# Optimization experiments

Hardware: AMD Instinct MI355X
Metric: run time of the kernel (lower is better)

The kernel has to match this reference:

```python
import jax, jax.numpy as jnp
import numpy as np

EPS_BN = 1e-5
EPS_SIM = 1e-8
PAD = 1
NUM_ITERS = 3


def capsule_conv2d(x, w):
    # x: [B, C, H, W]; w: [out_caps, in_caps, kh, kw, in_len, out_len]
    B, C, H, W = x.shape
    oc, ic, kh, kw, il, ol = w.shape
    # im2col patches, feature dim ordered (c, kh, kw) -> matches torch.unfold
    patches = jax.lax.conv_general_dilated_patches(
        x, (kh, kw), (1, 1), [(PAD, PAD), (PAD, PAD)])  # [B, C*kh*kw, H, W]
    N = H * W
    p = patches.reshape(B, ic, il, kh * kw, N)
    p = jnp.transpose(p, (0, 4, 1, 3, 2))  # [B, N, ic, kk, il]
    wf = w.reshape(oc, ic, kh * kw, il, ol)
    # per-patch capsule transform -> priors [B, N, oc, ic*kk, ol]
    priors = jnp.einsum('bnikl,oiklm->bnoikm', p, wf)
    priors = priors.reshape(B, N, oc, ic * kh * kw, ol)
    # k-means routing with Tonimoto similarity, 3 iterations, no squash
    out = priors.mean(axis=-2, keepdims=True)  # [B, N, oc, 1, ol]
    for _ in range(NUM_ITERS):
        dot = jnp.sum(priors * out, axis=-1, keepdims=True)
        n1 = jnp.sum(priors * priors, axis=-1, keepdims=True)
        n2 = jnp.sum(out * out, axis=-1, keepdims=True)
        logits = dot / jnp.maximum(n1 + n2 - dot, EPS_SIM)
        probs = jax.nn.softmax(logits, axis=-2)
        out = jnp.sum(probs * priors, axis=-2, keepdims=True)
    out = out[..., 0, :]                      # [B, N, oc, ol]
    out = out.reshape(B, H, W, oc * ol)       # channels = oc*ol
    return jnp.transpose(out, (0, 3, 1, 2))   # [B, C, H, W]


def batchnorm2d(x, gamma, beta):
    mean = x.mean(axis=(0, 2, 3), keepdims=True)
    var = x.var(axis=(0, 2, 3), keepdims=True)  # biased, as torch BN training fwd
    inv = jax.lax.rsqrt(var + EPS_BN)
    return gamma[None, :, None, None] * (x - mean) * inv + beta[None, :, None, None]


def setup_inputs() -> dict:
    key = jax.random.key(0)
    k0, k1, k2 = jax.random.split(key, 3)
    B, C, H, W = 2, 64, 96, 96
    IL = OL = 8
    x = jax.random.normal(k0, (B, C, H, W), jnp.float32)
    w1 = jax.random.normal(k1, (C // OL, C // IL, 3, 3, IL, OL), jnp.float32) * 0.1
    w2 = jax.random.normal(k2, (C // OL, C // OL, 3, 3, OL, OL), jnp.float32) * 0.1
    g1 = jnp.ones((C,), jnp.float32)
    b1 = jnp.zeros((C,), jnp.float32)
    g2 = jnp.ones((C,), jnp.float32)
    b2 = jnp.zeros((C,), jnp.float32)
    return {"x": x, "w1": w1, "g1": g1, "b1": b1, "w2": w2, "g2": g2, "b2": b2}


def reference(x, w1, g1, b1, w2, g2, b2):
    r = batchnorm2d(capsule_conv2d(x, w1), g1, b1)
    r = batchnorm2d(capsule_conv2d(r, w2), g2, b2)
    return x + r
```

## Files before the change

### kernel.cpp

```cpp
#include <hip/hip_runtime.h>
#include <hip/hip_bf16.h>

#define HW 9216
#define NPC 18432
#define NELEM 1179648
#define XSTR 72
#define PATCH_B 7776
#define XREC 12
#define XBUF_B (4*2*16*2*XREC*4)

typedef __attribute__((ext_vector_type(2))) float f32x2;
typedef __attribute__((ext_vector_type(4))) float f32x4v;
typedef __attribute__((ext_vector_type(8))) short short8v;

__device__ __forceinline__ int detect_is32(const unsigned short* __restrict__ w1u) {
    int lane = threadIdx.x & 63;
    int bad = 0;
    #pragma unroll
    for (int i = 0; i < 16; ++i) {
        unsigned short u = (unsigned short)(w1u[lane + i * 64] & 0x7FFF);
        bad |= (u >= 0x42C8);
    }
    return (__ballot(bad) != 0ULL) ? 1 : 0;
}

__device__ __forceinline__ float load_in(const void* p, int idx, int is32) {
    return is32 ? ((const float*)p)[idx]
                : __bfloat162float(((const __hip_bfloat16*)p)[idx]);
}

__device__ __forceinline__ float lo16(unsigned v) { return __int_as_float((int)(v << 16)); }
__device__ __forceinline__ float hi16(unsigned v) { return __int_as_float((int)(v & 0xFFFF0000u)); }
__device__ __forceinline__ unsigned pk2bf(float a, float b) {
    __hip_bfloat162 h = __float22bfloat162_rn(float2{a, b});
    return *(unsigned*)&h;
}

__device__ __forceinline__ float dotsq4(const f32x4v a) {
    float t = a[0] * a[0];
    t = fmaf(a[1], a[1], t);
    t = fmaf(a[2], a[2], t);
    t = fmaf(a[3], a[3], t);
    return t;
}
__device__ __forceinline__ float dot4(const f32x4v a, const float om[4]) {
    float t = a[0] * om[0];
    t = fmaf(a[1], om[1], t);
    t = fmaf(a[2], om[2], t);
    t = fmaf(a[3], om[3], t);
    return t;
}

__launch_bounds__(256)
__global__ void prep_kernel(const void* __restrict__ x,
                            const void* __restrict__ w1, const void* __restrict__ w2,
                            __hip_bfloat16* __restrict__ xt,
                            __hip_bfloat16* __restrict__ Bfr1,
                            __hip_bfloat16* __restrict__ Bfr2,
                            float* __restrict__ statz) {
    __shared__ float tile[64 * 33];
    const int bid = blockIdx.x;
    if (bid < 576) {
        const int is32 = detect_is32((const unsigned short*)w1);
        int xb = bid % 3, y = (bid / 3) % 96, b = bid / 288;
        int x0 = xb * 32;
        for (int e = threadIdx.x; e < 2048; e += 256) {
            int xl = e & 31, c = e >> 5;
            tile[c * 33 + xl] = load_in(x, ((b * 64 + c) * 96 + y) * 96 + x0 + xl, is32);
        }
        __syncthreads();
        for (int f = threadIdx.x; f < 1024; f += 256) {
            int c2 = f & 31, xl = f >> 5;
            float a = tile[(2 * c2) * 33 + xl];
            float c = tile[(2 * c2 + 1) * 33 + xl];
            *(unsigned*)&xt[((b * 96 + y) * 96 + x0 + xl) * 64 + 2 * c2] = pk2bf(a, c);
        }
    } else if (bid < 720) {
        const int is32 = detect_is32((const unsigned short*)w1);
        int t = (bid - 576) * 256 + threadIdx.x;
        int layer = t / 18432;
        int r = t - layer * 18432;
        int lane = r & 63;
        int fi = r >> 6;
        int h = fi & 1, g = (fi >> 1) & 1;
        int kq = fi >> 2;
        int k = kq % 9, o = kq / 9;
        int dy = k / 3, dx = k % 3;
        int quad = lane >> 4, colhi = (lane >> 3) & 1, m = lane & 7;
        int heff = h ^ (m >> 2);
        int act = (quad == 2 * heff + colhi);
        int i = g * 4 + 2 * heff + colhi;
        const void* w = layer ? w2 : w1;
        __hip_bfloat16* dst = layer ? Bfr2 : Bfr1;
        #pragma unroll
        for (int j = 0; j < 8; ++j) {
            float v = act ? load_in(w, ((((o * 8 + i) * 3 + dy) * 3 + dx) * 8 + j) * 8 + m, is32)
                          : 0.f;
            dst[(fi * 64 + lane) * 8 + j] = __float2bfloat16(v);
        }
    } else {
        for (int e = threadIdx.x; e < 2048; e += 256) statz[e] = 0.f;
    }
}

__device__ __forceinline__ void xexchange(float* __restrict__ xbufF, int slot,
                                          int o2w, int pos16, int g, int quad,
                                          int mhalf, float ac[4], float& se) {
    float* rec = xbufF + ((((slot * 2 + o2w) * 16 + pos16) * 2 + g) * XREC);
    if (quad < 2) {
        *(float4*)(rec + quad * 4) = make_float4(ac[0], ac[1], ac[2], ac[3]);
        if (quad == 0) rec[8] = se;
    }
    __syncthreads();
    const float* prec = xbufF + ((((slot * 2 + o2w) * 16 + pos16) * 2 + (1 - g)) * XREC);
    float4 po = *(const float4*)(prec + mhalf * 4);
    ac[0] += po.x; ac[1] += po.y; ac[2] += po.z; ac[3] += po.w;
    se += prec[8];
}

__launch_bounds__(256, 4)
__global__ void caps_kernel(const __hip_bfloat16* __restrict__ in,
                            const float* __restrict__ statPrev,
                            const void* __restrict__ gamma, const void* __restrict__ beta,
                            const void* __restrict__ wdt,
                            const __hip_bfloat16* __restrict__ Bfr,
                            __hip_bfloat16* __restrict__ yout,
                            float* __restrict__ statL,
                            int layer1) {
    __shared__ __align__(16) unsigned char smem[PATCH_B + XBUF_B];
    __hip_bfloat16* patchH = (__hip_bfloat16*)smem;
    float* xbufF = (float*)(smem + PATCH_B);
    float* omF = (float*)smem;
    float* scL = (float*)(smem + PATCH_B);
    float* shL = scL + 64;

    const int gx    = blockIdx.x;
    const int opair = gx & 3;
    const int x0    = (gx >> 2) * 16;
    const int y  = blockIdx.y;
    const int b  = blockIdx.z;
    const int tid = threadIdx.x;

    if (!layer1) {
        if (tid < 64) {
            const int is32 = detect_is32((const unsigned short*)wdt);
            int c = tid;
            float s = 0.f, ss = 0.f;
            #pragma unroll
            for (int cp = 0; cp < 8; ++cp) {
                s  += statPrev[cp * 128 + c];
                ss += statPrev[cp * 128 + 64 + c];
            }
            float mean = s * (1.f / (float)NPC);
            float var  = fmaxf(ss * (1.f / (float)NPC) - mean * mean, 0.f);
            float inv  = rsqrtf(var + 1e-5f);
            float g = load_in(gamma, c, is32) * inv;
            scL[c] = g;
            shL[c] = load_in(beta, c, is32) - mean * g;
        }
        __syncthreads();
    }

    for (int e = tid; e < 864; e += 256) {
        int c4 = e & 15;
        int q  = e >> 4;
        int xo = q % 18, row = q / 18;
        int yy = y + row - 1, xx = x0 + xo - 1;
        uint2 v = {0u, 0u};
        if (yy >= 0 && yy < 96 && xx >= 0 && xx < 96) {
            v = *(const uint2*)&in[((b * 96 + yy) * 96 + xx) * 64 + c4 * 4];
            if (!layer1) {
                int c = c4 * 4;
                float f0 = lo16(v.x) * scL[c]     + shL[c];
                float f1 = hi16(v.x) * scL[c + 1] + shL[c + 1];
                float f2 = lo16(v.y) * scL[c + 2] + shL[c + 2];
                float f3 = hi16(v.y) * scL[c + 3] + shL[c + 3];
                v.x = pk2bf(f0, f1);
                v.y = pk2bf(f2, f3);
            }
        }
        *(uint2*)&patchH[q * XSTR + c4 * 4] = v;
    }
    __syncthreads();

    const int lane  = tid & 63;
    const int wv    = tid >> 6;
    const int o2w   = wv >> 1;
    const int g     = wv & 1;
    const int pos16 = lane & 15;
    const int quad  = lane >> 4;
    const int mhalf = quad & 1;

    f32x4v P[9][2];
    {
        const int o = opair * 2 + o2w;
        #pragma unroll
        for (int k = 0; k < 9; ++k) {
            const int dy = k / 3, dx = k % 3;
            short8v a = *(const short8v*)&patchH[(dy * 18 + dx + pos16) * XSTR + g * 32 + quad * 8];
            #pragma unroll
            for (int h = 0; h < 2; ++h) {
                short8v bf = *(const short8v*)&Bfr[((((o * 9 + k) * 2 + g) * 2 + h) * 64 + lane) * 8];
                P[k][h] = __builtin_amdgcn_mfma_f32_16x16x32_bf16(bf, a, (f32x4v){0.f, 0.f, 0.f, 0.f}, 0, 0, 0);
            }
        }
    }
    #pragma unroll
    for (int k = 0; k < 9; ++k) {
        asm("" : "+v"(P[k][0]));
        asm("" : "+v"(P[k][1]));
    }

    float n1o[9];
    #pragma unroll
    for (int k = 0; k < 9; ++k) {
        float np1 = dotsq4(P[k][1]);
        n1o[k] = dotsq4(P[k][0]) + __shfl_xor(np1, 16, 64);
    }

    float om[4];
    {
        float ac[4];
        #pragma unroll
        for (int r = 0; r < 4; ++r) {
            float s = 0.f;
            #pragma unroll
            for (int k = 0; k < 9; ++k) s += P[k][0][r] + P[k][1][r];
            s += __shfl_xor(s, 32, 64);
            ac[r] = s;
        }
        float dummy = 0.f;
        xexchange(xbufF, 0, o2w, pos16, g, quad, mhalf, ac, dummy);
        #pragma unroll
        for (int r = 0; r < 4; ++r) om[r] = ac[r] * (1.f / 72.f);
    }
    float n2;
    {
        float n2p = dotsq4((f32x4v){om[0], om[1], om[2], om[3]});
        n2 = n2p + __shfl_xor(n2p, 16, 64);
    }

    #pragma unroll
    for (int it = 0; it < 3; ++it) {
        float se = 0.f;
        float ac[4] = {0.f, 0.f, 0.f, 0.f};
        #pragma unroll
        for (int k = 0; k < 9; ++k) {
            float dp0 = dot4(P[k][0], om);
            float dp1 = dot4(P[k][1], om);
            float d = dp0 + __shfl_xor(dp1, 16, 64);
            float denom = fmaxf(n1o[k] + n2 - d, 1e-8f);
            float e = __expf(d * __builtin_amdgcn_rcpf(denom));
            se += e;
            float eo = __shfl_xor(e, 16, 64);
            ac[0] = fmaf(e, P[k][0][0], fmaf(eo, P[k][1][0], ac[0]));
            ac[1] = fmaf(e, P[k][0][1], fmaf(eo, P[k][1][1], ac[1]));
            ac[2] = fmaf(e, P[k][0][2], fmaf(eo, P[k][1][2], ac[2]));
            ac[3] = fmaf(e, P[k][0][3], fmaf(eo, P[k][1][3], ac[3]));
        }
        se += __shfl_xor(se, 16, 64);
        se += __shfl_xor(se, 32, 64);
        #pragma unroll
        for (int r = 0; r < 4; ++r) ac[r] += __shfl_xor(ac[r], 32, 64);
        xexchange(xbufF, 1 + it, o2w, pos16, g, quad, mhalf, ac, se);
        float inv = __builtin_amdgcn_rcpf(se);
        #pragma unroll
        for (int r = 0; r < 4; ++r) om[r] = ac[r] * inv;
        float n2p = dotsq4((f32x4v){om[0], om[1], om[2], om[3]});
        n2 = n2p + __shfl_xor(n2p, 16, 64);
    }

    if (g == 0 && quad < 2) {
        const int o = opair * 2 + o2w;
        uint2 pk;
        pk.x = pk2bf(om[0], om[1]);
        pk.y = pk2bf(om[2], om[3]);
        *(uint2*)&yout[((b * 96 + y) * 96 + x0 + pos16) * 64 + o * 8 + mhalf * 4] = pk;
        *(float4*)&omF[(o2w * 16 + pos16) * 8 + mhalf * 4] = make_float4(om[0], om[1], om[2], om[3]);
    }
    __syncthreads();

    if (tid < 32) {
        int c16 = tid & 15, sel = tid >> 4;
        int oo2 = c16 >> 3, m = c16 & 7;
        float v = 0.f;
        #pragma unroll
        for (int pp = 0; pp < 16; ++pp) {
            float t = omF[(oo2 * 16 + pp) * 8 + m];
            v += sel ? t * t : t;
        }
        int cp = (blockIdx.x + blockIdx.y * 3 + blockIdx.z) & 7;
        atomicAdd(&statL[cp * 128 + sel * 64 + (opair * 2 + oo2) * 8 + m], v);
    }
}

__launch_bounds__(256)
__global__ void final_kernel(const void* __restrict__ xin,
                             const __hip_bfloat16* __restrict__ yt2,
                             const float* __restrict__ statL,
                             const void* __restrict__ gamma, const void* __restrict__ beta,
                             const void* __restrict__ w1,
                             void* __restrict__ outp) {
    __shared__ float tile[64 * 33];
    __shared__ float scL[64], shL[64];
    const int is32 = detect_is32((const unsigned short*)w1);
    if (threadIdx.x < 64) {
        int c = threadIdx.x;
        float s = 0.f, ss = 0.f;
        #pragma unroll
        for (int cp = 0; cp < 8; ++cp) {
            s  += statL[cp * 128 + c];
            ss += statL[cp * 128 + 64 + c];
        }
        float mean = s * (1.f / (float)NPC);
        float var  = fmaxf(ss * (1.f / (float)NPC) - mean * mean, 0.f);
        float inv  = rsqrtf(var + 1e-5f);
        float g = load_in(gamma, c, is32) * inv;
        scL[c] = g;
        shL[c] = load_in(beta, c, is32) - mean * g;
    }
    __syncthreads();

    int x0 = blockIdx.x * 32, y = blockIdx.y, b = blockIdx.z;
    for (int e = threadIdx.x; e < 1024; e += 256) {
        int c2 = e & 31, xl = e >> 5;
        unsigned v = *(const unsigned*)&yt2[((b * 96 + y) * 96 + x0 + xl) * 64 + c2 * 2];
        int c = c2 * 2;
        tile[c * 33 + xl]       = lo16(v) * scL[c]     + shL[c];
        tile[(c + 1) * 33 + xl] = hi16(v) * scL[c + 1] + shL[c + 1];
    }
    __syncthreads();
    for (int f = threadIdx.x; f < 2048; f += 256) {
        int xl = f & 31, c = f >> 5;
        int idx = ((b * 64 + c) * 96 + y) * 96 + x0 + xl;
        float v = load_in(xin, idx, is32) + tile[c * 33 + xl];
        if (is32) ((float*)outp)[idx] = v;
        else      ((__hip_bfloat16*)outp)[idx] = __float2bfloat16(v);
    }
}

extern "C" void kernel_launch(void* const* d_in, const int* in_sizes, int n_in,
                              void* d_out, int out_size, void* d_ws, size_t ws_size,
                              hipStream_t stream) {
    const void* x  = d_in[0];
    const void* w1 = d_in[1];
    const void* g1 = d_in[2];
    const void* b1 = d_in[3];
    const void* w2 = d_in[4];
    const void* g2 = d_in[5];
    const void* b2 = d_in[6];

    __hip_bfloat16* bufA = (__hip_bfloat16*)d_ws;
    __hip_bfloat16* bufB = bufA + NELEM;
    __hip_bfloat16* Bfr1 = bufB + NELEM;
    __hip_bfloat16* Bfr2 = Bfr1 + 147456;
    float* statz = (float*)(Bfr2 + 147456);
    float* statL1 = statz;
    float* statL2 = statz + 1024;

    prep_kernel<<<721, 256, 0, stream>>>(x, w1, w2, bufA, Bfr1, Bfr2, statz);

    dim3 cgrid(24, 96, 2);
    caps_kernel<<<cgrid, 256, 0, stream>>>(bufA, nullptr, nullptr, nullptr, w1,
                                           Bfr1, bufB, statL1, 1);
    caps_kernel<<<cgrid, 256, 0, stream>>>(bufB, statL1, g1, b1, w1,
                                           Bfr2, bufA, statL2, 0);
    final_kernel<<<dim3(3, 96, 2), 256, 0, stream>>>(x, bufA, statL2, g2, b2, w1, d_out);
}
```

Before: 160.8 us.

## Relayout weight fragments so each lane holds all eight output components

Changes the packed weight-fragment layout so that the MFMA output places all 8 output-length components of a position/input pair in one lane, split across the two h halves. The routing loop then computes dot products, norms and weighted accumulation lane-locally, dropping the per-k cross-lane shuffles for dp1 and e. In exchange, the final reductions shuffle 8 accumulators over two xor steps instead of 4 over one, and the exchange and store now write 8 floats.

New measurement: 176.8 us. 9.9% more time.

```diff
diff --git a/kernel.cpp b/kernel.cpp
--- a/kernel.cpp
+++ b/kernel.cpp
@@ -41,13 +41,6 @@
     t = fmaf(a[1], a[1], t);
     t = fmaf(a[2], a[2], t);
     t = fmaf(a[3], a[3], t);
-    return t;
-}
-__device__ __forceinline__ float dot4(const f32x4v a, const float om[4]) {
-    float t = a[0] * om[0];
-    t = fmaf(a[1], om[1], t);
-    t = fmaf(a[2], om[2], t);
-    t = fmaf(a[3], om[3], t);
     return t;
 }
 
@@ -86,10 +79,13 @@
         int kq = fi >> 2;
         int k = kq % 9, o = kq / 9;
         int dy = k / 3, dx = k % 3;
-        int quad = lane >> 4, colhi = (lane >> 3) & 1, m = lane & 7;
-        int heff = h ^ (m >> 2);
-        int act = (quad == 2 * heff + colhi);
-        int i = g * 4 + 2 * heff + colhi;
+        int quadA = lane >> 4;
+        int row = lane & 15;
+        int qD = row >> 2;
+        int il = 2 * (qD & 1) + (qD >> 1);
+        int act = (quadA == il);
+        int i = g * 4 + il;
+        int m = 4 * h + (row & 3);
         const void* w = layer ? w2 : w1;
         __hip_bfloat16* dst = layer ? Bfr2 : Bfr1;
         #pragma unroll
@@ -103,18 +99,21 @@
     }
 }
 
-__device__ __forceinline__ void xexchange(float* __restrict__ xbufF, int slot,
-                                          int o2w, int pos16, int g, int quad,
-                                          int mhalf, float ac[4], float& se) {
+__device__ __forceinline__ void xexchange8(float* __restrict__ xbufF, int slot,
+                                           int o2w, int pos16, int g, int quad,
+                                           float ac[8], float& se) {
     float* rec = xbufF + ((((slot * 2 + o2w) * 16 + pos16) * 2 + g) * XREC);
-    if (quad < 2) {
-        *(float4*)(rec + quad * 4) = make_float4(ac[0], ac[1], ac[2], ac[3]);
-        if (quad == 0) rec[8] = se;
+    if (quad == 0) {
+        *(float4*)(rec)     = make_float4(ac[0], ac[1], ac[2], ac[3]);
+        *(float4*)(rec + 4) = make_float4(ac[4], ac[5], ac[6], ac[7]);
+        rec[8] = se;
     }
     __syncthreads();
     const float* prec = xbufF + ((((slot * 2 + o2w) * 16 + pos16) * 2 + (1 - g)) * XREC);
-    float4 po = *(const float4*)(prec + mhalf * 4);
-    ac[0] += po.x; ac[1] += po.y; ac[2] += po.z; ac[3] += po.w;
+    float4 pa = *(const float4*)(prec);
+    float4 pb = *(const float4*)(prec + 4);
+    ac[0] += pa.x; ac[1] += pa.y; ac[2] += pa.z; ac[3] += pa.w;
+    ac[4] += pb.x; ac[5] += pb.y; ac[6] += pb.z; ac[7] += pb.w;
     se += prec[8];
 }
 
@@ -189,7 +188,6 @@
     const int g     = wv & 1;
     const int pos16 = lane & 15;
     const int quad  = lane >> 4;
-    const int mhalf = quad & 1;
 
     f32x4v P[9][2];
     {
@@ -212,71 +210,90 @@
     }
 
     float n1o[9];
+    float s2[8] = {0.f, 0.f, 0.f, 0.f, 0.f, 0.f, 0.f, 0.f};
     #pragma unroll
     for (int k = 0; k < 9; ++k) {
-        float np1 = dotsq4(P[k][1]);
-        n1o[k] = dotsq4(P[k][0]) + __shfl_xor(np1, 16, 64);
-    }
-
-    float om[4];
+        n1o[k] = dotsq4(P[k][0]) + dotsq4(P[k][1]);
+        #pragma unroll
+        for (int r = 0; r < 4; ++r) {
+            s2[r]     += P[k][0][r];
+            s2[4 + r] += P[k][1][r];
+        }
+    }
+
+    float om[8];
     {
-        float ac[4];
-        #pragma unroll
-        for (int r = 0; r < 4; ++r) {
-            float s = 0.f;
-            #pragma unroll
-            for (int k = 0; k < 9; ++k) s += P[k][0][r] + P[k][1][r];
-            s += __shfl_xor(s, 32, 64);
-            ac[r] = s;
+        float ac[8];
+        #pragma unroll
+        for (int r = 0; r < 8; ++r) {
+            float t = s2[r];
+            t += __shfl_xor(t, 16, 64);
+            t += __shfl_xor(t, 32, 64);
+            ac[r] = t;
         }
         float dummy = 0.f;
-        xexchange(xbufF, 0, o2w, pos16, g, quad, mhalf, ac, dummy);
-        #pragma unroll
-        for (int r = 0; r < 4; ++r) om[r] = ac[r] * (1.f / 72.f);
+        xexchange8(xbufF, 0, o2w, pos16, g, quad, ac, dummy);
+        #pragma unroll
+        for (int r = 0; r < 8; ++r) om[r] = ac[r] * (1.f / 72.f);
     }
     float n2;
     {
-        float n2p = dotsq4((f32x4v){om[0], om[1], om[2], om[3]});
-        n2 = n2p + __shfl_xor(n2p, 16, 64);
+        float t = om[0] * om[0];
+        #pragma unroll
+        for (int r = 1; r < 8; ++r) t = fmaf(om[r], om[r], t);
+        n2 = t;
     }
 
     #pragma unroll
     for (int it = 0; it < 3; ++it) {
         float se = 0.f;
-        float ac[4] = {0.f, 0.f, 0.f, 0.f};
+        float ac[8] = {0.f, 0.f, 0.f, 0.f, 0.f, 0.f, 0.f, 0.f};
         #pragma unroll
         for (int k = 0; k < 9; ++k) {
-            float dp0 = dot4(P[k][0], om);
-            float dp1 = dot4(P[k][1], om);
-            float d = dp0 + __shfl_xor(dp1, 16, 64);
+            float d = P[k][0][0] * om[0];
+            d = fmaf(P[k][0][1], om[1], d);
+            d = fmaf(P[k][0][2], om[2], d);
+            d = fmaf(P[k][0][3], om[3], d);
+            d = fmaf(P[k][1][0], om[4], d);
+            d = fmaf(P[k][1][1], om[5], d);
+            d = fmaf(P[k][1][2], om[6], d);
+            d = fmaf(P[k][1][3], om[7], d);
             float denom = fmaxf(n1o[k] + n2 - d, 1e-8f);
             float e = __expf(d * __builtin_amdgcn_rcpf(denom));
             se += e;
-            float eo = __shfl_xor(e, 16, 64);
-            ac[0] = fmaf(e, P[k][0][0], fmaf(eo, P[k][1][0], ac[0]));
-            ac[1] = fmaf(e, P[k][0][1], fmaf(eo, P[k][1][1], ac[1]));
-            ac[2] = fmaf(e, P[k][0][2], fmaf(eo, P[k][1][2], ac[2]));
-            ac[3] = fmaf(e, P[k][0][3], fmaf(eo, P[k][1][3], ac[3]));
+            #pragma unroll
+            for (int r = 0; r < 4; ++r) {
+                ac[r]     = fmaf(e, P[k][0][r], ac[r]);
+                ac[4 + r] = fmaf(e, P[k][1][r], ac[4 + r]);
+            }
         }
         se += __shfl_xor(se, 16, 64);
         se += __shfl_xor(se, 32, 64);
         #pragma unroll
-        for (int r = 0; r < 4; ++r) ac[r] += __shfl_xor(ac[r], 32, 64);
-        xexchange(xbufF, 1 + it, o2w, pos16, g, quad, mhalf, ac, se);
+        for (int r = 0; r < 8; ++r) {
+            ac[r] += __shfl_xor(ac[r], 16, 64);
+            ac[r] += __shfl_xor(ac[r], 32, 64);
+        }
+        xexchange8(xbufF, 1 + it, o2w, pos16, g, quad, ac, se);
         float inv = __builtin_amdgcn_rcpf(se);
         #pragma unroll
-        for (int r = 0; r < 4; ++r) om[r] = ac[r] * inv;
-        float n2p = dotsq4((f32x4v){om[0], om[1], om[2], om[3]});
-        n2 = n2p + __shfl_xor(n2p, 16, 64);
-    }
-
-    if (g == 0 && quad < 2) {
+        for (int r = 0; r < 8; ++r) om[r] = ac[r] * inv;
+        float t = om[0] * om[0];
+        #pragma unroll
+        for (int r = 1; r < 8; ++r) t = fmaf(om[r], om[r], t);
+        n2 = t;
+    }
+
+    if (g == 0 && quad == 0) {
         const int o = opair * 2 + o2w;
-        uint2 pk;
+        uint4 pk;
         pk.x = pk2bf(om[0], om[1]);
         pk.y = pk2bf(om[2], om[3]);
-        *(uint2*)&yout[((b * 96 + y) * 96 + x0 + pos16) * 64 + o * 8 + mhalf * 4] = pk;
-        *(float4*)&omF[(o2w * 16 + pos16) * 8 + mhalf * 4] = make_float4(om[0], om[1], om[2], om[3]);
+        pk.z = pk2bf(om[4], om[5]);
+        pk.w = pk2bf(om[6], om[7]);
+        *(uint4*)&yout[((b * 96 + y) * 96 + x0 + pos16) * 64 + o * 8] = pk;
+        *(float4*)&omF[(o2w * 16 + pos16) * 8]     = make_float4(om[0], om[1], om[2], om[3]);
+        *(float4*)&omF[(o2w * 16 + pos16) * 8 + 4] = make_float4(om[4], om[5], om[6], om[7]);
     }
     __syncthreads();
 
```
